# Kernel tuning notes

Measured on AMD Instinct MI355X. Metric: run time of the kernel, lower is better.

The kernel has to match this reference:

```python
import jax, jax.numpy as jnp
import numpy as np

D_MODEL = 1024
H = 16
D_K = D_MODEL // H


def setup_inputs() -> dict:
    key = jax.random.key(0)
    ks = jax.random.split(key, 9)
    s = 0.02
    x = jax.random.normal(ks[0], (2, 2048, D_MODEL), dtype=jnp.float32)
    Wq = jax.random.normal(ks[1], (D_MODEL, D_MODEL), dtype=jnp.float32) * s
    bq = jax.random.normal(ks[2], (D_MODEL,), dtype=jnp.float32) * s
    Wk = jax.random.normal(ks[3], (D_MODEL, D_MODEL), dtype=jnp.float32) * s
    bk = jax.random.normal(ks[4], (D_MODEL,), dtype=jnp.float32) * s
    Wv = jax.random.normal(ks[5], (D_MODEL, D_MODEL), dtype=jnp.float32) * s
    bv = jax.random.normal(ks[6], (D_MODEL,), dtype=jnp.float32) * s
    Wo = jax.random.normal(ks[7], (D_MODEL, D_MODEL), dtype=jnp.float32) * s
    bo = jax.random.normal(ks[8], (D_MODEL,), dtype=jnp.float32) * s
    return {"x": x, "Wq": Wq, "bq": bq, "Wk": Wk, "bk": bk,
            "Wv": Wv, "bv": bv, "Wo": Wo, "bo": bo}


def reference(x, Wq, bq, Wk, bk, Wv, bv, Wo, bo):
    b, s, _ = x.shape
    scale = 1.0 / jnp.sqrt(jnp.float32(D_K))
    # projections; [b, s, d] -> [b, h, s, d_k]
    def split_heads(t):
        return t.reshape(b, s, H, D_K).transpose(0, 2, 1, 3)
    q = split_heads(x @ Wq + bq)
    k = split_heads(x @ Wk + bk)
    v = split_heads(x @ Wv + bv)
    scores = jnp.einsum('bhqd,bhkd->bhqk', q, k) * scale  # [b,h,s,s]
    attn = jax.nn.softmax(scores, axis=-1)
    ctx = jnp.einsum('bhqk,bhkd->bhqd', attn, v)
    ctx = ctx.transpose(0, 2, 1, 3).reshape(b, s, D_MODEL)
    return ctx @ Wo + bo + x
```

## Files before the change

kernel.cpp:

```cpp
#include <hip/hip_runtime.h>
#include <hip/hip_bf16.h>
#include <stdint.h>

#define D_MODEL 1024
#define NH 16
#define DK 64
#define S_LEN 2048

typedef __attribute__((ext_vector_type(8))) __bf16 bf16x8;
typedef __attribute__((ext_vector_type(4))) float f32x4;

#define GLOBAL_AS __attribute__((address_space(1)))
#define LDS_AS    __attribute__((address_space(3)))

__device__ __forceinline__ void async16(const ushort* g, ushort* l) {
    __builtin_amdgcn_global_load_lds(
        (const GLOBAL_AS uint32_t*)(uintptr_t)(const void*)g,
        (LDS_AS uint32_t*)(uint32_t)(uintptr_t)(void*)l,
        16, 0, 0);
}

template <int N>
__device__ __forceinline__ void pipe_barrier() {
    asm volatile("s_waitcnt vmcnt(%0)\n\ts_barrier" :: "n"(N) : "memory");
}

__device__ __forceinline__ float fast_exp2(float x) {
    float r;
    asm("v_exp_f32 %0, %1" : "=v"(r) : "v"(x));
    return r;
}

__device__ __forceinline__ ushort f2bf(float f) {
    union { float f; uint32_t u; } v; v.f = f;
    uint32_t lsb = (v.u >> 16) & 1u;
    return (ushort)((v.u + 0x7fffu + lsb) >> 16);
}

__device__ __forceinline__ uint32_t packbf(float a, float b) {
    union { float f; uint32_t u; } x, y; x.f = a; y.f = b;
    return ((x.u + 0x8000u) >> 16) | ((y.u + 0x8000u) & 0xffff0000u);
}

__device__ __forceinline__ uint32_t packbf_rn(float a, float b) {
    union { __hip_bfloat162 h; uint32_t u; } cv;
    cv.h = __float22bfloat162_rn(make_float2(a, b));
    return cv.u;
}

__device__ __forceinline__ bf16x8 ldfrag(const ushort* p) {
    union { uint4 u; bf16x8 b; } cv;
    cv.u = *(const uint4*)p;
    return cv.b;
}

__global__ void cvt_fused_kernel(
    const float* __restrict__ x, ushort* __restrict__ xb,
    const float* __restrict__ W0, const float* __restrict__ W1,
    const float* __restrict__ W2, const float* __restrict__ W3,
    ushort* __restrict__ D0, ushort* __restrict__ D1,
    ushort* __restrict__ D2, ushort* __restrict__ D3,
    const float* __restrict__ bq, const float* __restrict__ bk,
    const float* __restrict__ bv, float* __restrict__ biasq) {
    __shared__ float tile[32][33];
    const int bid = blockIdx.x, tid = threadIdx.x;
    if (bid < 4096) {
        int i = bid * 256 + tid;
        float4 v = ((const float4*)x)[i];
        ushort4 o;
        o.x = f2bf(v.x); o.y = f2bf(v.y); o.z = f2bf(v.z); o.w = f2bf(v.w);
        ((ushort4*)xb)[i] = o;
    } else if (bid < 8192) {
        int t = bid - 4096;
        int z = t >> 10, rem = t & 1023;
        const float* W; ushort* D;
        switch (z) {
            case 0: W = W0; D = D0; break;
            case 1: W = W1; D = D1; break;
            case 2: W = W2; D = D2; break;
            default: W = W3; D = D3; break;
        }
        int by = (rem >> 5) * 32, bx = (rem & 31) * 32;
        int tx = tid & 31, ty = tid >> 5;
#pragma unroll
        for (int j = 0; j < 32; j += 8)
            tile[ty + j][tx] = W[(size_t)(by + ty + j) * D_MODEL + bx + tx];
        __syncthreads();
#pragma unroll
        for (int j = 0; j < 32; j += 8)
            D[(size_t)(bx + ty + j) * D_MODEL + by + tx] = f2bf(tile[tx][ty + j]);
    } else {
        int i = (bid - 8192) * 256 + tid;
        float v = (i < 1024) ? bq[i] : (i < 2048 ? bk[i - 1024] : bv[i - 2048]);
        biasq[i] = v;
    }
}

template <int MODE>
__global__ __launch_bounds__(256, 3) void gemm_kernel(
    const ushort* __restrict__ A, const ushort* __restrict__ Bt,
    const float* __restrict__ bias,
    ushort* __restrict__ outQ, ushort* __restrict__ outK, ushort* __restrict__ outVt,
    const float* __restrict__ xres, float* __restrict__ outF) {
    constexpr int BN = (MODE == 0) ? 128 : 64;
    constexpr int NI = (MODE == 0) ? 4 : 2;
    constexpr int NS = (MODE == 0) ? 4 : 3;
    constexpr int ABUF = 4096;
    constexpr int BBUF = (MODE == 0) ? 4096 : 2048;
    constexpr int SMEM = (MODE == 0) ? 24576 : 18432;
    __shared__ __align__(16) ushort smem[SMEM];
    ushort* sAb = smem;
    ushort* sBb = smem + 3 * ABUF;

    const int tid = threadIdx.x;
    const int wave = tid >> 6, lane = tid & 63;
    const int lr = lane & 15, lq = lane >> 4;
    const int srow = lane >> 3, sp = lane & 7;

    const int bid = blockIdx.x;
    const int xcd = bid & 7, lb = bid >> 3;
    int bx, by;
    if (MODE == 0) { bx = xcd * 3 + (lb % 3); by = lb / 3; }
    else           { by = xcd * 4 + (lb & 3); bx = lb >> 2; }
    const int blockM = by * 128;
    const int blockN = bx * BN;
    const int waveM = (wave >> 1) * 64;
    const int waveN = (MODE == 0) ? (wave & 1) * 64 : (wave & 1) * 32;

    auto stage = [&](int k0, int buf) {
        ushort* a = sAb + buf * ABUF;
#pragma unroll
        for (int t = 0; t < 2; t++) {
            int Rb = wave * 16 + t * 8;
            int R = Rb + srow;
            int L = sp ^ (R & 7);
            int m = 2 * R + (L >> 2);
            int kc = L & 3;
            async16(&A[(size_t)(blockM + m) * D_MODEL + k0 + kc * 8], a + Rb * 64);
        }
        ushort* b = sBb + buf * BBUF;
        if (MODE == 0) {
#pragma unroll
            for (int t = 0; t < 2; t++) {
                int Rb = wave * 16 + t * 8;
                int R = Rb + srow;
                int L = sp ^ (R & 7);
                int n = 2 * R + (L >> 2);
                int kc = L & 3;
                async16(&Bt[(size_t)(blockN + n) * D_MODEL + k0 + kc * 8], b + Rb * 64);
            }
        } else {
            int Rb = wave * 8;
            int R = Rb + srow;
            int L = sp ^ (R & 7);
            int n = 2 * R + (L >> 2);
            int kc = L & 3;
            async16(&Bt[(size_t)(blockN + n) * D_MODEL + k0 + kc * 8], b + Rb * 64);
        }
    };

    const int RA = (waveM >> 1) + (lr >> 1);
    const int offA = RA * 64 + ((((lr & 1) * 4 + lq) ^ (RA & 7)) * 8);
    const int RB = (waveN >> 1) + (lr >> 1);
    const int offB = RB * 64 + ((((lr & 1) * 4 + lq) ^ (RB & 7)) * 8);

    f32x4 acc[4][NI] = {};

    stage(0, 0);
    stage(32, 1);
    pipe_barrier<NS>();

#pragma unroll
    for (int k = 0; k < 32; k++) {
        const int buf = k % 3;
        if (k + 2 < 32) stage((k + 2) * 32, (k + 2) % 3);
        const ushort* a = sAb + buf * ABUF;
        const ushort* b = sBb + buf * BBUF;
        bf16x8 af[4], bfr[NI];
#pragma unroll
        for (int mi = 0; mi < 4; mi++)
            af[mi] = ldfrag(&a[offA + mi * 512]);
#pragma unroll
        for (int ni = 0; ni < NI; ni++)
            bfr[ni] = ldfrag(&b[offB + ni * 512]);
#pragma unroll
        for (int mi = 0; mi < 4; mi++)
#pragma unroll
            for (int ni = 0; ni < NI; ni++)
                acc[mi][ni] = __builtin_amdgcn_mfma_f32_16x16x32_bf16(
                    af[mi], bfr[ni], acc[mi][ni], 0, 0, 0);
        if (k < 30) pipe_barrier<NS>();
        else if (k == 30) pipe_barrier<0>();
    }
    __syncthreads();

    const int bglob = blockM >> 11;
    const int sbase = blockM & 2047;

    if (MODE == 0) {
        const int which = bx >> 3;
        if (which < 2) {
            const float scale = (which == 0) ? 0.1803368801f : 1.0f;
#pragma unroll
            for (int ni = 0; ni < 4; ni++) {
                const int n_loc = waveN + ni * 16 + lr;
                const float bn = bias[blockN + n_loc];
#pragma unroll
                for (int mi = 0; mi < 4; mi++)
#pragma unroll
                    for (int r = 0; r < 4; r++) {
                        int m_loc = waveM + mi * 16 + lq * 4 + r;
                        smem[m_loc * 136 + n_loc] =
                            f2bf((acc[mi][ni][r] + bn) * scale);
                    }
            }
            __syncthreads();
            ushort* outp = (which == 0) ? outQ : outK;
            const int hbase = (which == 0) ? bx * 2 : (bx - 8) * 2;
#pragma unroll
            for (int j = 0; j < 8; j++) {
                int c = tid + j * 256;
                int m = c >> 4, nc = c & 15;
                int hh = nc >> 3, d8 = nc & 7;
                uint4 w = *(uint4*)&smem[m * 136 + nc * 8];
                size_t bh = (size_t)(bglob * NH + hbase + hh);
                *(uint4*)&outp[(bh * S_LEN + sbase + m) * DK + d8 * 8] = w;
            }
        } else {
#pragma unroll
            for (int ni = 0; ni < 4; ni++) {
                const int n_loc = waveN + ni * 16 + lr;
                const float bn = bias[blockN + n_loc];
#pragma unroll
                for (int mi = 0; mi < 4; mi++) {
                    uint2 w;
                    w.x = packbf(acc[mi][ni][0] + bn, acc[mi][ni][1] + bn);
                    w.y = packbf(acc[mi][ni][2] + bn, acc[mi][ni][3] + bn);
                    int m_base = waveM + mi * 16 + lq * 4;
                    *(uint2*)&smem[n_loc * 136 + m_base] = w;
                }
            }
            __syncthreads();
            const int hbase = (bx - 16) * 2;
#pragma unroll
            for (int j = 0; j < 8; j++) {
                int c = tid + j * 256;
                int n_loc = c >> 4, m8 = c & 15;
                int d = n_loc & 63, hh = n_loc >> 6;
                uint4 w = *(uint4*)&smem[n_loc * 136 + m8 * 8];
                size_t bh = (size_t)(bglob * NH + hbase + hh);
                *(uint4*)&outVt[(bh * DK + d) * S_LEN + sbase + m8 * 8] = w;
            }
        }
    } else {
        float* sCf = (float*)smem;
#pragma unroll
        for (int ni = 0; ni < 2; ni++) {
            const int n_loc = waveN + ni * 16 + lr;
            const float bn = bias[blockN + n_loc];
#pragma unroll
            for (int mi = 0; mi < 4; mi++)
#pragma unroll
                for (int r = 0; r < 4; r++) {
                    int m_loc = waveM + mi * 16 + lq * 4 + r;
                    sCf[m_loc * 68 + n_loc] = acc[mi][ni][r] + bn;
                }
        }
        __syncthreads();
#pragma unroll
        for (int j = 0; j < 8; j++) {
            int c = tid + j * 256;
            int m = c >> 4, nc = c & 15;
            float4 v = *(float4*)&sCf[m * 68 + nc * 4];
            size_t idx = (size_t)(blockM + m) * D_MODEL + blockN + nc * 4;
            float4 xr = *(const float4*)&xres[idx];
            v.x += xr.x; v.y += xr.y; v.z += xr.z; v.w += xr.w;
            *(float4*)&outF[idx] = v;
        }
    }
}

__global__ __launch_bounds__(256, 2) void attn_kernel(
    const ushort* __restrict__ Q, const ushort* __restrict__ Km,
    const ushort* __restrict__ Vt, ushort* __restrict__ ctx) {
    const int bid = blockIdx.x;
    const int xcd = bid & 7, lb = bid >> 3;
    const int bh = xcd * 4 + (lb & 3);
    const int qt = lb >> 2;
    const int q0 = qt * 128;
    __shared__ __align__(16) ushort sK[3][64 * 64];
    __shared__ __align__(16) ushort sV[3][64 * 64];
    __shared__ __align__(16) ushort sQP[4][32 * 64];
    const int tid = threadIdx.x;
    const int wave = tid >> 6, lane = tid & 63;
    const int lr = lane & 15, lq = lane >> 4;
    const int srow = lane >> 3, sp = lane & 7;
    const ushort* Qh = Q + (size_t)bh * S_LEN * DK;
    const ushort* Kh = Km + (size_t)bh * S_LEN * DK;
    const ushort* Vh = Vt + (size_t)bh * DK * S_LEN;
    ushort* sPw = sQP[wave];

#pragma unroll
    for (int t = 0; t < 4; t++) {
        int row = t * 8 + srow;
        int c = sp ^ (row & 7);
        async16(&Qh[(size_t)(q0 + wave * 32 + row) * DK + c * 8],
                &sPw[t * 8 * 64]);
    }

    auto stageK = [&](int k0, int buf) {
#pragma unroll
        for (int t = 0; t < 2; t++) {
            int row = wave * 16 + t * 8 + srow;
            int c = sp ^ (row & 7);
            async16(&Kh[(size_t)(k0 + row) * DK + c * 8],
                    &sK[buf][(wave * 16 + t * 8) * 64]);
        }
    };
    auto stageV = [&](int k0, int buf) {
#pragma unroll
        for (int t = 0; t < 2; t++) {
            int row = wave * 16 + t * 8 + srow;
            int c = sp ^ (row & 7);
            async16(&Vh[(size_t)row * S_LEN + k0 + c * 8],
                    &sV[buf][(wave * 16 + t * 8) * 64]);
        }
    };

    stageK(0, 0);
    stageV(0, 0);
    stageK(64, 1);
    stageV(64, 1);
    stageK(128, 2);
    __syncthreads();

    bf16x8 qf[2][2];
#pragma unroll
    for (int nj = 0; nj < 2; nj++)
#pragma unroll
        for (int kk = 0; kk < 2; kk++)
            qf[nj][kk] = ldfrag(&sPw[(nj * 16 + lr) * 64 +
                                     (((kk * 4 + lq) ^ (lr & 7)) * 8)]);

    union { uint4 u; bf16x8 b; } one_u;
    one_u.u = make_uint4(0x3F803F80u, 0x3F803F80u, 0x3F803F80u, 0x3F803F80u);
    const bf16x8 ones = one_u.b;

    f32x4 cacc[2][4] = {};
    f32x4 ssum[2] = {};

    auto qk = [&](const ushort* sk, f32x4 (*sacc)[2]) {
#pragma unroll
        for (int kk = 0; kk < 2; kk++) {
            bf16x8 kf[4];
            int swz = ((kk * 4 + lq) ^ (lr & 7)) * 8;
#pragma unroll
            for (int mi = 0; mi < 4; mi++)
                kf[mi] = ldfrag(&sk[(mi * 16 + lr) * 64 + swz]);
            __builtin_amdgcn_s_setprio(1);
#pragma unroll
            for (int mi = 0; mi < 4; mi++)
#pragma unroll
                for (int nj = 0; nj < 2; nj++)
                    sacc[mi][nj] = __builtin_amdgcn_mfma_f32_16x16x32_bf16(
                        kf[mi], qf[nj][kk], sacc[mi][nj], 0, 0, 0);
            __builtin_amdgcn_s_setprio(0);
        }
    };

    auto expP = [&](f32x4 (*sacc)[2]) {
#pragma unroll
        for (int mi = 0; mi < 4; mi++)
#pragma unroll
            for (int nj = 0; nj < 2; nj++) {
                float p0 = fast_exp2(sacc[mi][nj][0]);
                float p1 = fast_exp2(sacc[mi][nj][1]);
                float p2 = fast_exp2(sacc[mi][nj][2]);
                float p3 = fast_exp2(sacc[mi][nj][3]);
                uint2 w;
                w.x = packbf_rn(p0, p1);
                w.y = packbf_rn(p2, p3);
                int physc = (mi * 2 + (lq >> 1)) ^ (lr & 7);
                *(uint2*)&sPw[(nj * 16 + lr) * 64 + physc * 8 + (lq & 1) * 4] = w;
            }
    };

    auto pv = [&](const ushort* sv) {
#pragma unroll
        for (int ks = 0; ks < 2; ks++) {
            bf16x8 pf[2], vf[4];
            int swz = ((ks * 4 + lq) ^ (lr & 7)) * 8;
#pragma unroll
            for (int nj = 0; nj < 2; nj++)
                pf[nj] = ldfrag(&sPw[(nj * 16 + lr) * 64 + swz]);
#pragma unroll
            for (int nd = 0; nd < 4; nd++)
                vf[nd] = ldfrag(&sv[(nd * 16 + lr) * 64 + swz]);
            __builtin_amdgcn_s_setprio(1);
#pragma unroll
            for (int nj = 0; nj < 2; nj++)
#pragma unroll
                for (int nd = 0; nd < 4; nd++)
                    cacc[nj][nd] = __builtin_amdgcn_mfma_f32_16x16x32_bf16(
                        pf[nj], vf[nd], cacc[nj][nd], 0, 0, 0);
#pragma unroll
            for (int nj = 0; nj < 2; nj++)
                ssum[nj] = __builtin_amdgcn_mfma_f32_16x16x32_bf16(
                    pf[nj], ones, ssum[nj], 0, 0, 0);
            __builtin_amdgcn_s_setprio(0);
        }
    };

    {
        f32x4 s0[4][2] = {};
        qk(sK[0], s0);
        expP(s0);
    }
    __builtin_amdgcn_s_barrier();

#pragma unroll 3
    for (int k = 0; k < 31; k++) {
        if (k + 3 < 32) stageK((k + 3) * 64, (k + 3) % 3);
        if (k + 2 < 32) stageV((k + 2) * 64, (k + 2) % 3);
        f32x4 s2[4][2] = {};
        qk(sK[(k + 1) % 3], s2);
        pv(sV[k % 3]);
        if (k < 29) pipe_barrier<4>();
        else if (k == 29) pipe_barrier<2>();
        else pipe_barrier<0>();
        expP(s2);
    }
    pv(sV[31 % 3]);

    const int b = bh >> 4, h = bh & 15;
    float inv[2][4];
#pragma unroll
    for (int nj = 0; nj < 2; nj++)
#pragma unroll
        for (int r = 0; r < 4; r++)
            inv[nj][r] = __builtin_amdgcn_rcpf(ssum[nj][r]);
#pragma unroll
    for (int nj = 0; nj < 2; nj++)
#pragma unroll
        for (int nd = 0; nd < 4; nd++)
#pragma unroll
            for (int r = 0; r < 4; r++) {
                int qrow = q0 + wave * 32 + nj * 16 + lq * 4 + r;
                int d = nd * 16 + lr;
                float v = cacc[nj][nd][r] * inv[nj][r];
                ctx[(size_t)(b * S_LEN + qrow) * D_MODEL + h * DK + d] = f2bf(v);
            }
}


extern "C" void kernel_launch(void* const* d_in, const int* in_sizes, int n_in,
                              void* d_out, int out_size, void* d_ws, size_t ws_size,
                              hipStream_t stream) {
    const float* x  = (const float*)d_in[0];
    const float* Wq = (const float*)d_in[1];
    const float* bq = (const float*)d_in[2];
    const float* Wk = (const float*)d_in[3];
    const float* bk = (const float*)d_in[4];
    const float* Wv = (const float*)d_in[5];
    const float* bv = (const float*)d_in[6];
    const float* Wo = (const float*)d_in[7];
    const float* bo = (const float*)d_in[8];

    char* ws = (char*)d_ws;
    ushort* xb    = (ushort*)(ws);
    ushort* wqkv  = (ushort*)(ws + (8ull  << 20));
    ushort* wo_t  = (ushort*)(ws + (14ull << 20));
    ushort* qbuf  = (ushort*)(ws + (16ull << 20));
    ushort* kbuf  = (ushort*)(ws + (24ull << 20));
    ushort* vtb   = (ushort*)(ws + (32ull << 20));
    ushort* ctx   = (ushort*)(ws + (40ull << 20));
    float*  biasq = (float*)(ws + (48ull << 20));

    cvt_fused_kernel<<<8204, 256, 0, stream>>>(
        x, xb, Wq, Wk, Wv, Wo,
        wqkv, wqkv + 1024 * 1024, wqkv + 2 * 1024 * 1024, wo_t,
        bq, bk, bv, biasq);

    gemm_kernel<0><<<768, 256, 0, stream>>>(
        xb, wqkv, biasq, qbuf, kbuf, vtb, nullptr, nullptr);
    attn_kernel<<<512, 256, 0, stream>>>(qbuf, kbuf, vtb, ctx);
    gemm_kernel<1><<<512, 256, 0, stream>>>(
        ctx, wo_t, bo, nullptr, nullptr, nullptr, x, (float*)d_out);
}
```

Measured before the change: 186.7 us.

## Switch attention to 32x32x16 MFMA with register-resident P via permlane swap

Rewrites the attention inner loop to use 32x32x16 bf16 MFMAs, computing S transposed so the exponentiated P tile can be repacked in registers with v_permlane32_swap and fed straight into the PV MFMA. This removes the LDS round-trip for P and the extra MFMAs against a ones vector for the row sum. The row sum is now accumulated with VALU adds and combined across half-waves at the end. The output store also writes packed 8-byte chunks per lane. It relies on correct lane/register layout of the 32x32 MFMA outputs, and the softmax still has no max subtraction, as before.

```diff
diff --git a/kernel.cpp b/kernel.cpp
--- a/kernel.cpp
+++ b/kernel.cpp
@@ -9,6 +9,7 @@
 
 typedef __attribute__((ext_vector_type(8))) __bf16 bf16x8;
 typedef __attribute__((ext_vector_type(4))) float f32x4;
+typedef __attribute__((ext_vector_type(16))) float f32x16;
 
 #define GLOBAL_AS __attribute__((address_space(1)))
 #define LDS_AS    __attribute__((address_space(3)))
@@ -293,7 +294,7 @@
     __shared__ __align__(16) ushort sQP[4][32 * 64];
     const int tid = threadIdx.x;
     const int wave = tid >> 6, lane = tid & 63;
-    const int lr = lane & 15, lq = lane >> 4;
+    const int l31 = lane & 31, hi = lane >> 5;
     const int srow = lane >> 3, sp = lane & 7;
     const ushort* Qh = Q + (size_t)bh * S_LEN * DK;
     const ushort* Kh = Km + (size_t)bh * S_LEN * DK;
@@ -334,85 +335,72 @@
     stageK(128, 2);
     __syncthreads();
 
-    bf16x8 qf[2][2];
-#pragma unroll
-    for (int nj = 0; nj < 2; nj++)
-#pragma unroll
-        for (int kk = 0; kk < 2; kk++)
-            qf[nj][kk] = ldfrag(&sPw[(nj * 16 + lr) * 64 +
-                                     (((kk * 4 + lq) ^ (lr & 7)) * 8)]);
-
-    union { uint4 u; bf16x8 b; } one_u;
-    one_u.u = make_uint4(0x3F803F80u, 0x3F803F80u, 0x3F803F80u, 0x3F803F80u);
-    const bf16x8 ones = one_u.b;
-
-    f32x4 cacc[2][4] = {};
-    f32x4 ssum[2] = {};
-
-    auto qk = [&](const ushort* sk, f32x4 (*sacc)[2]) {
-#pragma unroll
-        for (int kk = 0; kk < 2; kk++) {
-            bf16x8 kf[4];
-            int swz = ((kk * 4 + lq) ^ (lr & 7)) * 8;
-#pragma unroll
-            for (int mi = 0; mi < 4; mi++)
-                kf[mi] = ldfrag(&sk[(mi * 16 + lr) * 64 + swz]);
+    bf16x8 qf[4];
+#pragma unroll
+    for (int kk = 0; kk < 4; kk++)
+        qf[kk] = ldfrag(&sPw[l31 * 64 + (((2 * kk + hi) ^ (l31 & 7)) * 8)]);
+
+    f32x16 cacc[2] = {};
+    bf16x8 pfreg[4];
+    float ssum_part = 0.0f;
+
+    auto qk = [&](const ushort* sk, f32x16* sacc) {
+#pragma unroll
+        for (int kk = 0; kk < 4; kk++) {
+            bf16x8 kf0 = ldfrag(&sk[l31 * 64 + (((2 * kk + hi) ^ (l31 & 7)) * 8)]);
+            bf16x8 kf1 = ldfrag(&sk[(32 + l31) * 64 +
+                                    (((2 * kk + hi) ^ (l31 & 7)) * 8)]);
             __builtin_amdgcn_s_setprio(1);
-#pragma unroll
-            for (int mi = 0; mi < 4; mi++)
-#pragma unroll
-                for (int nj = 0; nj < 2; nj++)
-                    sacc[mi][nj] = __builtin_amdgcn_mfma_f32_16x16x32_bf16(
-                        kf[mi], qf[nj][kk], sacc[mi][nj], 0, 0, 0);
+            sacc[0] = __builtin_amdgcn_mfma_f32_32x32x16_bf16(
+                kf0, qf[kk], sacc[0], 0, 0, 0);
+            sacc[1] = __builtin_amdgcn_mfma_f32_32x32x16_bf16(
+                kf1, qf[kk], sacc[1], 0, 0, 0);
             __builtin_amdgcn_s_setprio(0);
         }
     };
 
-    auto expP = [&](f32x4 (*sacc)[2]) {
-#pragma unroll
-        for (int mi = 0; mi < 4; mi++)
-#pragma unroll
-            for (int nj = 0; nj < 2; nj++) {
-                float p0 = fast_exp2(sacc[mi][nj][0]);
-                float p1 = fast_exp2(sacc[mi][nj][1]);
-                float p2 = fast_exp2(sacc[mi][nj][2]);
-                float p3 = fast_exp2(sacc[mi][nj][3]);
-                uint2 w;
-                w.x = packbf_rn(p0, p1);
-                w.y = packbf_rn(p2, p3);
-                int physc = (mi * 2 + (lq >> 1)) ^ (lr & 7);
-                *(uint2*)&sPw[(nj * 16 + lr) * 64 + physc * 8 + (lq & 1) * 4] = w;
-            }
+    auto expP = [&](f32x16* sacc) {
+#pragma unroll
+        for (int w = 0; w < 4; w++) {
+            const int mi = w >> 1, r8 = (w & 1) * 8;
+            float e0 = fast_exp2(sacc[mi][r8 + 0]);
+            float e1 = fast_exp2(sacc[mi][r8 + 1]);
+            float e2 = fast_exp2(sacc[mi][r8 + 2]);
+            float e3 = fast_exp2(sacc[mi][r8 + 3]);
+            float e4 = fast_exp2(sacc[mi][r8 + 4]);
+            float e5 = fast_exp2(sacc[mi][r8 + 5]);
+            float e6 = fast_exp2(sacc[mi][r8 + 6]);
+            float e7 = fast_exp2(sacc[mi][r8 + 7]);
+            ssum_part += ((e0 + e1) + (e2 + e3)) + ((e4 + e5) + (e6 + e7));
+            uint32_t X0 = packbf_rn(e0, e1);
+            uint32_t X1 = packbf_rn(e2, e3);
+            uint32_t Y0 = packbf_rn(e4, e5);
+            uint32_t Y1 = packbf_rn(e6, e7);
+            asm("v_permlane32_swap_b32 %0, %1" : "+v"(X0), "+v"(Y0));
+            asm("v_permlane32_swap_b32 %0, %1" : "+v"(X1), "+v"(Y1));
+            union { uint4 u; bf16x8 b; } cv;
+            cv.u = make_uint4(X0, X1, Y0, Y1);
+            pfreg[w] = cv.b;
+        }
     };
 
     auto pv = [&](const ushort* sv) {
 #pragma unroll
-        for (int ks = 0; ks < 2; ks++) {
-            bf16x8 pf[2], vf[4];
-            int swz = ((ks * 4 + lq) ^ (lr & 7)) * 8;
-#pragma unroll
-            for (int nj = 0; nj < 2; nj++)
-                pf[nj] = ldfrag(&sPw[(nj * 16 + lr) * 64 + swz]);
-#pragma unroll
-            for (int nd = 0; nd < 4; nd++)
-                vf[nd] = ldfrag(&sv[(nd * 16 + lr) * 64 + swz]);
+        for (int w = 0; w < 4; w++) {
+            bf16x8 vf0 = ldfrag(&sv[l31 * 64 + (((2 * w + hi) ^ (l31 & 7)) * 8)]);
+            bf16x8 vf1 = ldfrag(&sv[(32 + l31) * 64 +
+                                    (((2 * w + hi) ^ (l31 & 7)) * 8)]);
             __builtin_amdgcn_s_setprio(1);
-#pragma unroll
-            for (int nj = 0; nj < 2; nj++)
-#pragma unroll
-                for (int nd = 0; nd < 4; nd++)
-                    cacc[nj][nd] = __builtin_amdgcn_mfma_f32_16x16x32_bf16(
-                        pf[nj], vf[nd], cacc[nj][nd], 0, 0, 0);
-#pragma unroll
-            for (int nj = 0; nj < 2; nj++)
-                ssum[nj] = __builtin_amdgcn_mfma_f32_16x16x32_bf16(
-                    pf[nj], ones, ssum[nj], 0, 0, 0);
+            cacc[0] = __builtin_amdgcn_mfma_f32_32x32x16_bf16(
+                vf0, pfreg[w], cacc[0], 0, 0, 0);
+            cacc[1] = __builtin_amdgcn_mfma_f32_32x32x16_bf16(
+                vf1, pfreg[w], cacc[1], 0, 0, 0);
             __builtin_amdgcn_s_setprio(0);
         }
     };
 
     {
-        f32x4 s0[4][2] = {};
+        f32x16 s0[2] = {};
         qk(sK[0], s0);
         expP(s0);
     }
@@ -422,7 +410,7 @@
     for (int k = 0; k < 31; k++) {
         if (k + 3 < 32) stageK((k + 3) * 64, (k + 3) % 3);
         if (k + 2 < 32) stageV((k + 2) * 64, (k + 2) % 3);
-        f32x4 s2[4][2] = {};
+        f32x16 s2[2] = {};
         qk(sK[(k + 1) % 3], s2);
         pv(sV[k % 3]);
         if (k < 29) pipe_barrier<4>();
@@ -432,24 +420,25 @@
     }
     pv(sV[31 % 3]);
 
+    float spp = ssum_part, tpp = ssum_part;
+    asm("v_permlane32_swap_b32 %0, %1" : "+v"(spp), "+v"(tpp));
+    float partner = hi ? spp : tpp;
+    float inv_q = __builtin_amdgcn_rcpf(ssum_part + partner);
+
     const int b = bh >> 4, h = bh & 15;
-    float inv[2][4];
-#pragma unroll
-    for (int nj = 0; nj < 2; nj++)
-#pragma unroll
-        for (int r = 0; r < 4; r++)
-            inv[nj][r] = __builtin_amdgcn_rcpf(ssum[nj][r]);
-#pragma unroll
-    for (int nj = 0; nj < 2; nj++)
-#pragma unroll
-        for (int nd = 0; nd < 4; nd++)
-#pragma unroll
-            for (int r = 0; r < 4; r++) {
-                int qrow = q0 + wave * 32 + nj * 16 + lq * 4 + r;
-                int d = nd * 16 + lr;
-                float v = cacc[nj][nd][r] * inv[nj][r];
-                ctx[(size_t)(b * S_LEN + qrow) * D_MODEL + h * DK + d] = f2bf(v);
-            }
+    const int qrow = q0 + wave * 32 + l31;
+    ushort* orow = ctx + (size_t)(b * S_LEN + qrow) * D_MODEL + h * DK;
+#pragma unroll
+    for (int nd = 0; nd < 2; nd++)
+#pragma unroll
+        for (int t = 0; t < 4; t++) {
+            uint2 wv;
+            wv.x = packbf_rn(cacc[nd][4 * t + 0] * inv_q,
+                             cacc[nd][4 * t + 1] * inv_q);
+            wv.y = packbf_rn(cacc[nd][4 * t + 2] * inv_q,
+                             cacc[nd][4 * t + 3] * inv_q);
+            *(uint2*)&orow[nd * 32 + 8 * t + 4 * hi] = wv;
+        }
 }
 
 
```

After: 533.3 us. 186% more time.
